# Optimization experiments

Measured on AMD Instinct MI355X. Metric: run time of the kernel, lower is better.

The kernel has to match this reference:

```python
import jax, jax.numpy as jnp
import numpy as np

N_NODES = 500000
N_EDGES = 16000000
F_DIM = 5


def setup_inputs() -> dict:
    key = jax.random.key(0)
    ks = jax.random.split(key, 20)
    inp = {
        "h": jax.random.normal(ks[0], (N_NODES, F_DIM), dtype=jnp.float32),
        "edge_index": jax.random.randint(ks[1], (2, N_EDGES), 0, N_NODES, dtype=jnp.int64),
        "edge_weight": jax.random.uniform(ks[2], (N_EDGES,), dtype=jnp.float32),
    }
    # GCNConv lin weights (bias=False in lin, conv has its own bias) x3
    s = 1.0 / np.sqrt(F_DIM)
    for i in range(3):
        inp[f"W{i+1}"] = jax.random.uniform(ks[3 + i], (F_DIM, F_DIM), jnp.float32, -s, s)
        inp[f"b{i+1}"] = jax.random.uniform(ks[6 + i], (F_DIM,), jnp.float32, -s, s)
    # fc1..fc3 Linear(5,5) with bias
    for i in range(3):
        inp[f"fcW{i+1}"] = jax.random.uniform(ks[9 + i], (F_DIM, F_DIM), jnp.float32, -s, s)
        inp[f"fcb{i+1}"] = jax.random.uniform(ks[12 + i], (F_DIM,), jnp.float32, -s, s)
    return inp


def _gcn_conv(h, src, dst, edge_weight, W, b, num_nodes):
    # lin transform (torch Linear: x @ W.T), no self loops, no normalization
    x = h @ W.T  # [N, F]
    # message: x_j * w_e, gathered from source nodes
    msg = x[src] * edge_weight[:, None]  # [E, F]
    # mean aggregation over target nodes
    agg = jax.ops.segment_sum(msg, dst, num_segments=num_nodes)  # [N, F]
    cnt = jax.ops.segment_sum(jnp.ones_like(edge_weight), dst, num_segments=num_nodes)
    agg = agg / jnp.maximum(cnt, 1.0)[:, None]
    return agg + b


def reference(h, edge_index, edge_weight, W1, b1, W2, b2, W3, b3,
              fcW1, fcb1, fcW2, fcb2, fcW3, fcb3):
    src, dst = edge_index[0], edge_index[1]
    n = h.shape[0]
    for W, b in ((W1, b1), (W2, b2), (W3, b3)):
        h = jax.nn.relu(_gcn_conv(h, src, dst, edge_weight, W, b, n))
    h = jax.nn.relu(h @ fcW1.T + fcb1)
    h = jax.nn.relu(h @ fcW2.T + fcb2)
    h = h @ fcW3.T + fcb3
    return h
```

## Files before the change

kernel.cpp:

```cpp
#include <hip/hip_runtime.h>
#include <hip/hip_fp16.h>


constexpr int N_NODES = 500000;
constexpr int N_EDGES = 16000000;
constexpr int F = 5;
constexpr int NPB = 1024;
constexpr int K_BKT = (N_NODES + NPB - 1) / NPB;
constexpr int CAP = 35008;
constexpr int PART_BLOCKS = 1024;
constexpr int CHUNK = N_EDGES / PART_BLOCKS;
constexpr int SUB = 3125;
constexpr int ACH = 4096;

__global__ void k_init(unsigned* __restrict__ gtail) {
    int b = blockIdx.x * blockDim.x + threadIdx.x;
    if (b < K_BKT) gtail[b] = (unsigned)(b * CAP);
}

__global__ __launch_bounds__(512) void k_part(const int* __restrict__ src,
                                              const int* __restrict__ dst,
                                              const float* __restrict__ ew,
                                              unsigned* __restrict__ gtail,
                                              uint2* __restrict__ sorted) {
    __shared__ uint2 stage[SUB];
    __shared__ unsigned short sbkt[SUB];
    __shared__ unsigned hcnt[512];
    __shared__ unsigned scn[512];
    __shared__ unsigned gb2[512];
    const int t = threadIdx.x;
    const int base_e = blockIdx.x * CHUNK;

#pragma unroll 1
    for (int rnd = 0; rnd < CHUNK / SUB; ++rnd) {
        const int sub_lo = base_e + rnd * SUB;
        hcnt[t] = 0;
        __syncthreads();
        for (int e = sub_lo + t; e < sub_lo + SUB; e += 512)
            atomicAdd(&hcnt[(unsigned)dst[e] >> 10], 1u);
        __syncthreads();
        scn[t] = hcnt[t];
        __syncthreads();
        for (int d = 1; d < 512; d <<= 1) {
            unsigned add = (t >= d) ? scn[t - d] : 0u;
            __syncthreads();
            scn[t] += add;
            __syncthreads();
        }
        unsigned cnt = hcnt[t];
        scn[t] -= cnt;
        if (t < K_BKT && cnt)
            gb2[t] = atomicAdd(&gtail[t], cnt) - scn[t];
        __syncthreads();
        hcnt[t] = 0;
        __syncthreads();
        for (int e = sub_lo + t; e < sub_lo + SUB; e += 512) {
            unsigned d = (unsigned)__builtin_nontemporal_load(dst + e);
            unsigned bkt = d >> 10;
            unsigned p = scn[bkt] + atomicAdd(&hcnt[bkt], 1u);
            uint2 pay;
            pay.x = (unsigned)__builtin_nontemporal_load(src + e) | ((d & (NPB - 1u)) << 19);
            pay.y = __float_as_uint(__builtin_nontemporal_load(ew + e));
            stage[p] = pay;
            sbkt[p] = (unsigned short)bkt;
        }
        __syncthreads();
        for (int p = t; p < SUB; p += 512)
            sorted[gb2[sbkt[p]] + p] = stage[p];
        __syncthreads();
    }
}

__device__ __forceinline__ uint4 pack5(const float o[F]) {
    __half2 p01 = __floats2half2_rn(o[0], o[1]);
    __half2 p23 = __floats2half2_rn(o[2], o[3]);
    __half2 p4z = __floats2half2_rn(o[4], 0.f);
    uint4 pk;
    pk.x = *(const unsigned*)&p01;
    pk.y = *(const unsigned*)&p23;
    pk.z = *(const unsigned*)&p4z;
    pk.w = 0u;
    return pk;
}

__global__ void k_lin(const float* __restrict__ h, const float* __restrict__ W,
                      uint4* __restrict__ x) {
    int i = blockIdx.x * blockDim.x + threadIdx.x;
    if (i >= N_NODES) return;
    float hv[F], o[F];
#pragma unroll
    for (int k = 0; k < F; ++k) hv[k] = h[i * F + k];
#pragma unroll
    for (int f = 0; f < F; ++f) {
        float acc = 0.f;
#pragma unroll
        for (int k = 0; k < F; ++k) acc = fmaf(hv[k], W[f * F + k], acc);
        o[f] = acc;
    }
    x[i] = pack5(o);
}

__device__ __forceinline__ void accum_bucket(const unsigned long long* __restrict__ sorted,
                                             unsigned lo, unsigned hi,
                                             const uint4* __restrict__ x,
                                             unsigned long long* __restrict__ stage,
                                             unsigned* __restrict__ cnt,
                                             unsigned* __restrict__ excl,
                                             unsigned* __restrict__ wsum,
                                             float acc[F], float& deg) {
    const int t = threadIdx.x;
    const int wid = t >> 6, lane = t & 63;
    for (unsigned cb = lo; cb < hi; cb += ACH) {
        const unsigned n = min((unsigned)ACH, hi - cb);
        cnt[t] = 0;
        __syncthreads();
        unsigned long long pe[4];
        unsigned dl[4], rk[4];
#pragma unroll
        for (int i = 0; i < 4; ++i) {
            unsigned idx = (unsigned)t + i * 1024u;
            if (idx < n) {
                pe[i] = __builtin_nontemporal_load(sorted + cb + idx);
                dl[i] = ((unsigned)pe[i]) >> 19;
                rk[i] = atomicAdd(&cnt[dl[i]], 1u);
            }
        }
        __syncthreads();
        unsigned c = cnt[t];
        unsigned inc = c;
#pragma unroll
        for (int d = 1; d < 64; d <<= 1) {
            unsigned up = __shfl_up(inc, d);
            if (lane >= d) inc += up;
        }
        if (lane == 63) wsum[wid] = inc;
        __syncthreads();
        unsigned wbase = 0;
#pragma unroll
        for (int wv = 0; wv < 15; ++wv)
            if (wv < wid) wbase += wsum[wv];
        unsigned my_excl = wbase + inc - c;
        excl[t] = my_excl;
        __syncthreads();
#pragma unroll
        for (int i = 0; i < 4; ++i) {
            unsigned idx = (unsigned)t + i * 1024u;
            if (idx < n) stage[excl[dl[i]] + rk[i]] = pe[i];
        }
        __syncthreads();
        deg += (float)c;
        for (unsigned i = 0; i < c; ++i) {
            unsigned long long e = stage[my_excl + i];
            unsigned px = (unsigned)e;
            float w = __uint_as_float((unsigned)(e >> 32));
            uint4 v = x[px & 0x7FFFFu];
            float2 f01 = __half22float2(*reinterpret_cast<const __half2*>(&v.x));
            float2 f23 = __half22float2(*reinterpret_cast<const __half2*>(&v.y));
            float2 f4z = __half22float2(*reinterpret_cast<const __half2*>(&v.z));
            acc[0] = fmaf(f01.x, w, acc[0]);
            acc[1] = fmaf(f01.y, w, acc[1]);
            acc[2] = fmaf(f23.x, w, acc[2]);
            acc[3] = fmaf(f23.y, w, acc[3]);
            acc[4] = fmaf(f4z.x, w, acc[4]);
        }
        __syncthreads();
    }
}

__global__ __launch_bounds__(1024) void k_gacc(const unsigned long long* __restrict__ sorted,
                                               const unsigned* __restrict__ gtail,
                                               const uint4* __restrict__ x,
                                               const float* __restrict__ bias,
                                               const float* __restrict__ Wn,
                                               uint4* __restrict__ xn) {
    __shared__ unsigned long long stage[ACH];
    __shared__ unsigned cnt[NPB];
    __shared__ unsigned excl[NPB];
    __shared__ unsigned wsum[16];
    float acc[F] = {0.f, 0.f, 0.f, 0.f, 0.f};
    float deg = 0.f;
    const unsigned b = blockIdx.x;
    accum_bucket(sorted, b * CAP, gtail[b], x, stage, cnt, excl, wsum, acc, deg);
    int node = b * NPB + threadIdx.x;
    if (node < N_NODES) {
        float inv = 1.0f / fmaxf(deg, 1.0f);
        float hv[F], o[F];
#pragma unroll
        for (int f = 0; f < F; ++f) hv[f] = fmaxf(fmaf(acc[f], inv, bias[f]), 0.f);
#pragma unroll
        for (int f = 0; f < F; ++f) {
            float s = 0.f;
#pragma unroll
            for (int kk = 0; kk < F; ++kk) s = fmaf(hv[kk], Wn[f * F + kk], s);
            o[f] = s;
        }
        xn[node] = pack5(o);
    }
}

__global__ __launch_bounds__(1024) void k_gfinal(const unsigned long long* __restrict__ sorted,
                                                 const unsigned* __restrict__ gtail,
                                                 const uint4* __restrict__ x,
                                                 const float* __restrict__ b3,
                                                 const float* __restrict__ fcW1, const float* __restrict__ fcb1,
                                                 const float* __restrict__ fcW2, const float* __restrict__ fcb2,
                                                 const float* __restrict__ fcW3, const float* __restrict__ fcb3,
                                                 float* __restrict__ out) {
    __shared__ unsigned long long stage[ACH];
    __shared__ unsigned cnt[NPB];
    __shared__ unsigned excl[NPB];
    __shared__ unsigned wsum[16];
    float acc[F] = {0.f, 0.f, 0.f, 0.f, 0.f};
    float deg = 0.f;
    const unsigned b = blockIdx.x;
    accum_bucket(sorted, b * CAP, gtail[b], x, stage, cnt, excl, wsum, acc, deg);
    int node = b * NPB + threadIdx.x;
    if (node < N_NODES) {
        float inv = 1.0f / fmaxf(deg, 1.0f);
        float h3[F], t1[F], t2[F];
#pragma unroll
        for (int f = 0; f < F; ++f) h3[f] = fmaxf(fmaf(acc[f], inv, b3[f]), 0.f);
#pragma unroll
        for (int f = 0; f < F; ++f) {
            float s = fcb1[f];
#pragma unroll
            for (int kk = 0; kk < F; ++kk) s = fmaf(h3[kk], fcW1[f * F + kk], s);
            t1[f] = fmaxf(s, 0.f);
        }
#pragma unroll
        for (int f = 0; f < F; ++f) {
            float s = fcb2[f];
#pragma unroll
            for (int kk = 0; kk < F; ++kk) s = fmaf(t1[kk], fcW2[f * F + kk], s);
            t2[f] = fmaxf(s, 0.f);
        }
#pragma unroll
        for (int f = 0; f < F; ++f) {
            float s = fcb3[f];
#pragma unroll
            for (int kk = 0; kk < F; ++kk) s = fmaf(t2[kk], fcW3[f * F + kk], s);
            out[node * F + f] = s;
        }
    }
}

extern "C" void kernel_launch(void* const* d_in, const int* in_sizes, int n_in,
                              void* d_out, int out_size, void* d_ws, size_t ws_size,
                              hipStream_t stream) {
    const float* h    = (const float*)d_in[0];
    const int*   ei   = (const int*)d_in[1];
    const float* ew   = (const float*)d_in[2];
    const float* W1   = (const float*)d_in[3];
    const float* b1   = (const float*)d_in[4];
    const float* W2   = (const float*)d_in[5];
    const float* b2   = (const float*)d_in[6];
    const float* W3   = (const float*)d_in[7];
    const float* b3   = (const float*)d_in[8];
    const float* fcW1 = (const float*)d_in[9];
    const float* fcb1 = (const float*)d_in[10];
    const float* fcW2 = (const float*)d_in[11];
    const float* fcb2 = (const float*)d_in[12];
    const float* fcW3 = (const float*)d_in[13];
    const float* fcb3 = (const float*)d_in[14];
    float* out = (float*)d_out;

    const int* srcp = ei;
    const int* dstp = ei + N_EDGES;

    char* ws = (char*)d_ws;
    const size_t MiB = 1024 * 1024;
    unsigned* gtail   = (unsigned*)(ws + 0);
    uint4*    xA      = (uint4*)(ws + 1 * MiB);
    uint4*    xB      = (uint4*)(ws + 10 * MiB);
    uint2*    sorted  = (uint2*)(ws + 19 * MiB);
    const unsigned long long* sorted64 = (const unsigned long long*)sorted;

    dim3 gn((N_NODES + 255) / 256);

    k_init<<<1, 512, 0, stream>>>(gtail);
    k_part<<<PART_BLOCKS, 512, 0, stream>>>(srcp, dstp, ew, gtail, sorted);

    k_lin<<<gn, 256, 0, stream>>>(h, W1, xA);
    k_gacc<<<K_BKT, 1024, 0, stream>>>(sorted64, gtail, xA, b1, W2, xB);
    k_gacc<<<K_BKT, 1024, 0, stream>>>(sorted64, gtail, xB, b2, W3, xA);
    k_gfinal<<<K_BKT, 1024, 0, stream>>>(sorted64, gtail, xA, b3,
                                         fcW1, fcb1, fcW2, fcb2, fcW3, fcb3, out);
}
```

Measured before the change: 934.1 us.

## Build per-node CSR once and use thread-per-node gather for all layers

Adds a second sorting pass that orders each destination bucket's edges by node and records per-node offset and count. All three aggregation layers then use a simple thread-per-node gather over contiguous edges instead of redoing a shared-memory counting sort in every layer. This removes repeated per-layer sorting and atomics. It costs an extra full read and write of the edge array, needs a larger workspace, and per-thread strided edge reads are less coalesced.

```diff
diff --git a/kernel.cpp b/kernel.cpp
--- a/kernel.cpp
+++ b/kernel.cpp
@@ -12,6 +12,7 @@
 constexpr int CHUNK = N_EDGES / PART_BLOCKS;
 constexpr int SUB = 3125;
 constexpr int ACH = 4096;
+constexpr int ACC_BLOCKS = (N_NODES + 255) / 256;
 
 __global__ void k_init(unsigned* __restrict__ gtail) {
     int b = blockIdx.x * blockDim.x + threadIdx.x;
@@ -71,6 +72,69 @@
     }
 }
 
+__global__ __launch_bounds__(1024) void k_sort2(const unsigned long long* __restrict__ in,
+                                                const unsigned* __restrict__ gtail,
+                                                uint2* __restrict__ nodeoff,
+                                                unsigned long long* __restrict__ out) {
+    __shared__ unsigned cnt[NPB];
+    __shared__ unsigned excl[NPB];
+    __shared__ unsigned wsum[16];
+    const int t = threadIdx.x;
+    const int wid = t >> 6, lane = t & 63;
+    const unsigned b = blockIdx.x;
+    const unsigned lo = b * CAP, hi = gtail[b];
+    cnt[t] = 0;
+    __syncthreads();
+    for (unsigned e = lo + t; e < hi; e += 1024) {
+        unsigned long long pe = __builtin_nontemporal_load(in + e);
+        atomicAdd(&cnt[((unsigned)pe) >> 19], 1u);
+    }
+    __syncthreads();
+    unsigned c = cnt[t];
+    unsigned inc = c;
+#pragma unroll
+    for (int d = 1; d < 64; d <<= 1) {
+        unsigned up = __shfl_up(inc, d);
+        if (lane >= d) inc += up;
+    }
+    if (lane == 63) wsum[wid] = inc;
+    __syncthreads();
+    unsigned wbase = 0;
+#pragma unroll
+    for (int wv = 0; wv < 15; ++wv)
+        if (wv < wid) wbase += wsum[wv];
+    unsigned my_excl = wbase + inc - c;
+    excl[t] = my_excl;
+    int node = (int)(b * NPB) + t;
+    if (node < N_NODES) nodeoff[node] = make_uint2(lo + my_excl, c);
+    __syncthreads();
+    cnt[t] = 0;
+    __syncthreads();
+    unsigned e = lo + t;
+    for (; e + 3072 < hi; e += 4096) {
+        unsigned long long p0 = __builtin_nontemporal_load(in + e);
+        unsigned long long p1 = __builtin_nontemporal_load(in + e + 1024);
+        unsigned long long p2 = __builtin_nontemporal_load(in + e + 2048);
+        unsigned long long p3 = __builtin_nontemporal_load(in + e + 3072);
+        unsigned d0 = ((unsigned)p0) >> 19, d1 = ((unsigned)p1) >> 19;
+        unsigned d2 = ((unsigned)p2) >> 19, d3 = ((unsigned)p3) >> 19;
+        unsigned q0 = excl[d0] + atomicAdd(&cnt[d0], 1u);
+        unsigned q1 = excl[d1] + atomicAdd(&cnt[d1], 1u);
+        unsigned q2 = excl[d2] + atomicAdd(&cnt[d2], 1u);
+        unsigned q3 = excl[d3] + atomicAdd(&cnt[d3], 1u);
+        out[lo + q0] = p0;
+        out[lo + q1] = p1;
+        out[lo + q2] = p2;
+        out[lo + q3] = p3;
+    }
+    for (; e < hi; e += 1024) {
+        unsigned long long p0 = __builtin_nontemporal_load(in + e);
+        unsigned d0 = ((unsigned)p0) >> 19;
+        unsigned q0 = excl[d0] + atomicAdd(&cnt[d0], 1u);
+        out[lo + q0] = p0;
+    }
+}
+
 __device__ __forceinline__ uint4 pack5(const float o[F]) {
     __half2 p01 = __floats2half2_rn(o[0], o[1]);
     __half2 p23 = __floats2half2_rn(o[2], o[3]);
@@ -98,6 +162,109 @@
         o[f] = acc;
     }
     x[i] = pack5(o);
+}
+
+__device__ __forceinline__ void fma_edge(unsigned long long pe, const uint4& v,
+                                         float acc[F]) {
+    float w = __uint_as_float((unsigned)(pe >> 32));
+    float2 f01 = __half22float2(*reinterpret_cast<const __half2*>(&v.x));
+    float2 f23 = __half22float2(*reinterpret_cast<const __half2*>(&v.y));
+    float2 f4z = __half22float2(*reinterpret_cast<const __half2*>(&v.z));
+    acc[0] = fmaf(f01.x, w, acc[0]);
+    acc[1] = fmaf(f01.y, w, acc[1]);
+    acc[2] = fmaf(f23.x, w, acc[2]);
+    acc[3] = fmaf(f23.y, w, acc[3]);
+    acc[4] = fmaf(f4z.x, w, acc[4]);
+}
+
+__device__ __forceinline__ void node_accum(const unsigned long long* __restrict__ s2,
+                                           uint2 oc, const uint4* __restrict__ x,
+                                           float acc[F]) {
+    unsigned i = 0;
+    for (; i + 4 <= oc.y; i += 4) {
+        unsigned long long e0 = s2[oc.x + i];
+        unsigned long long e1 = s2[oc.x + i + 1];
+        unsigned long long e2 = s2[oc.x + i + 2];
+        unsigned long long e3 = s2[oc.x + i + 3];
+        uint4 v0 = x[(unsigned)e0 & 0x7FFFFu];
+        uint4 v1 = x[(unsigned)e1 & 0x7FFFFu];
+        uint4 v2 = x[(unsigned)e2 & 0x7FFFFu];
+        uint4 v3 = x[(unsigned)e3 & 0x7FFFFu];
+        fma_edge(e0, v0, acc);
+        fma_edge(e1, v1, acc);
+        fma_edge(e2, v2, acc);
+        fma_edge(e3, v3, acc);
+    }
+    for (; i < oc.y; ++i) {
+        unsigned long long e0 = s2[oc.x + i];
+        uint4 v0 = x[(unsigned)e0 & 0x7FFFFu];
+        fma_edge(e0, v0, acc);
+    }
+}
+
+__global__ __launch_bounds__(256) void k_gacc2(const unsigned long long* __restrict__ s2,
+                                               const uint2* __restrict__ nodeoff,
+                                               const uint4* __restrict__ x,
+                                               const float* __restrict__ bias,
+                                               const float* __restrict__ Wn,
+                                               uint4* __restrict__ xn) {
+    int node = blockIdx.x * 256 + threadIdx.x;
+    if (node >= N_NODES) return;
+    uint2 oc = nodeoff[node];
+    float acc[F] = {0.f, 0.f, 0.f, 0.f, 0.f};
+    node_accum(s2, oc, x, acc);
+    float inv = 1.0f / fmaxf((float)oc.y, 1.0f);
+    float hv[F], o[F];
+#pragma unroll
+    for (int f = 0; f < F; ++f) hv[f] = fmaxf(fmaf(acc[f], inv, bias[f]), 0.f);
+#pragma unroll
+    for (int f = 0; f < F; ++f) {
+        float s = 0.f;
+#pragma unroll
+        for (int kk = 0; kk < F; ++kk) s = fmaf(hv[kk], Wn[f * F + kk], s);
+        o[f] = s;
+    }
+    xn[node] = pack5(o);
+}
+
+__global__ __launch_bounds__(256) void k_gfinal2(const unsigned long long* __restrict__ s2,
+                                                 const uint2* __restrict__ nodeoff,
+                                                 const uint4* __restrict__ x,
+                                                 const float* __restrict__ b3,
+                                                 const float* __restrict__ fcW1, const float* __restrict__ fcb1,
+                                                 const float* __restrict__ fcW2, const float* __restrict__ fcb2,
+                                                 const float* __restrict__ fcW3, const float* __restrict__ fcb3,
+                                                 float* __restrict__ out) {
+    int node = blockIdx.x * 256 + threadIdx.x;
+    if (node >= N_NODES) return;
+    uint2 oc = nodeoff[node];
+    float acc[F] = {0.f, 0.f, 0.f, 0.f, 0.f};
+    node_accum(s2, oc, x, acc);
+    float inv = 1.0f / fmaxf((float)oc.y, 1.0f);
+    float h3[F], t1[F], t2[F];
+#pragma unroll
+    for (int f = 0; f < F; ++f) h3[f] = fmaxf(fmaf(acc[f], inv, b3[f]), 0.f);
+#pragma unroll
+    for (int f = 0; f < F; ++f) {
+        float s = fcb1[f];
+#pragma unroll
+        for (int kk = 0; kk < F; ++kk) s = fmaf(h3[kk], fcW1[f * F + kk], s);
+        t1[f] = fmaxf(s, 0.f);
+    }
+#pragma unroll
+    for (int f = 0; f < F; ++f) {
+        float s = fcb2[f];
+#pragma unroll
+        for (int kk = 0; kk < F; ++kk) s = fmaf(t1[kk], fcW2[f * F + kk], s);
+        t2[f] = fmaxf(s, 0.f);
+    }
+#pragma unroll
+    for (int f = 0; f < F; ++f) {
+        float s = fcb3[f];
+#pragma unroll
+        for (int kk = 0; kk < F; ++kk) s = fmaf(t2[kk], fcW3[f * F + kk], s);
+        out[node * F + f] = s;
+    }
 }
 
 __device__ __forceinline__ void accum_bucket(const unsigned long long* __restrict__ sorted,
@@ -269,20 +436,33 @@
 
     char* ws = (char*)d_ws;
     const size_t MiB = 1024 * 1024;
+    const size_t SORT_BYTES = (size_t)K_BKT * CAP * 8;
     unsigned* gtail   = (unsigned*)(ws + 0);
     uint4*    xA      = (uint4*)(ws + 1 * MiB);
     uint4*    xB      = (uint4*)(ws + 10 * MiB);
-    uint2*    sorted  = (uint2*)(ws + 19 * MiB);
+    uint2*    nodeoff = (uint2*)(ws + 18 * MiB);
+    uint2*    sorted  = (uint2*)(ws + 22 * MiB);
+    unsigned long long* sorted2 =
+        (unsigned long long*)(ws + 153 * MiB);
     const unsigned long long* sorted64 = (const unsigned long long*)sorted;
+    const size_t NEED = 153 * MiB + SORT_BYTES;
 
     dim3 gn((N_NODES + 255) / 256);
 
     k_init<<<1, 512, 0, stream>>>(gtail);
     k_part<<<PART_BLOCKS, 512, 0, stream>>>(srcp, dstp, ew, gtail, sorted);
-
     k_lin<<<gn, 256, 0, stream>>>(h, W1, xA);
-    k_gacc<<<K_BKT, 1024, 0, stream>>>(sorted64, gtail, xA, b1, W2, xB);
-    k_gacc<<<K_BKT, 1024, 0, stream>>>(sorted64, gtail, xB, b2, W3, xA);
-    k_gfinal<<<K_BKT, 1024, 0, stream>>>(sorted64, gtail, xA, b3,
-                                         fcW1, fcb1, fcW2, fcb2, fcW3, fcb3, out);
-}
+
+    if (ws_size >= NEED) {
+        k_sort2<<<K_BKT, 1024, 0, stream>>>(sorted64, gtail, nodeoff, sorted2);
+        k_gacc2<<<ACC_BLOCKS, 256, 0, stream>>>(sorted2, nodeoff, xA, b1, W2, xB);
+        k_gacc2<<<ACC_BLOCKS, 256, 0, stream>>>(sorted2, nodeoff, xB, b2, W3, xA);
+        k_gfinal2<<<ACC_BLOCKS, 256, 0, stream>>>(sorted2, nodeoff, xA, b3,
+                                                  fcW1, fcb1, fcW2, fcb2, fcW3, fcb3, out);
+    } else {
+        k_gacc<<<K_BKT, 1024, 0, stream>>>(sorted64, gtail, xA, b1, W2, xB);
+        k_gacc<<<K_BKT, 1024, 0, stream>>>(sorted64, gtail, xB, b2, W3, xA);
+        k_gfinal<<<K_BKT, 1024, 0, stream>>>(sorted64, gtail, xA, b3,
+                                             fcW1, fcb1, fcW2, fcb2, fcW3, fcb3, out);
+    }
+}
```

Result: slower. 1.382 ms (+48.0%).

## Prefetch next edge chunk during local sort and unroll gather loop by four

Applied to the files above, without the earlier changes.

The per-bucket accumulation now loads the next chunk of sorted edges into registers while the current chunk is being scattered into shared memory. It also unrolls the per-node gather loop four ways so four x loads are in flight at once. Chunk size grows from 4096 to 6144 edges, the partition grid is set to 1000 blocks of 4000 sub-chunks, and the count and prefix arrays share one shared-memory buffer. The extra registers for six prefetched edges plus the unrolled loads raise register pressure, and the larger stage uses more LDS, both of which can cut occupancy.

```diff
diff --git a/kernel.cpp b/kernel.cpp
--- a/kernel.cpp
+++ b/kernel.cpp
@@ -8,10 +8,10 @@
 constexpr int NPB = 1024;
 constexpr int K_BKT = (N_NODES + NPB - 1) / NPB;
 constexpr int CAP = 35008;
-constexpr int PART_BLOCKS = 1024;
+constexpr int PART_BLOCKS = 1000;
 constexpr int CHUNK = N_EDGES / PART_BLOCKS;
-constexpr int SUB = 3125;
-constexpr int ACH = 4096;
+constexpr int SUB = 4000;
+constexpr int ACH = 6144;
 
 __global__ void k_init(unsigned* __restrict__ gtail) {
     int b = blockIdx.x * blockDim.x + threadIdx.x;
@@ -100,33 +100,51 @@
     x[i] = pack5(o);
 }
 
+__device__ __forceinline__ void fma_edge(unsigned long long pe, const uint4& v,
+                                         float acc[F]) {
+    float w = __uint_as_float((unsigned)(pe >> 32));
+    float2 f01 = __half22float2(*reinterpret_cast<const __half2*>(&v.x));
+    float2 f23 = __half22float2(*reinterpret_cast<const __half2*>(&v.y));
+    float2 f4z = __half22float2(*reinterpret_cast<const __half2*>(&v.z));
+    acc[0] = fmaf(f01.x, w, acc[0]);
+    acc[1] = fmaf(f01.y, w, acc[1]);
+    acc[2] = fmaf(f23.x, w, acc[2]);
+    acc[3] = fmaf(f23.y, w, acc[3]);
+    acc[4] = fmaf(f4z.x, w, acc[4]);
+}
+
 __device__ __forceinline__ void accum_bucket(const unsigned long long* __restrict__ sorted,
                                              unsigned lo, unsigned hi,
                                              const uint4* __restrict__ x,
                                              unsigned long long* __restrict__ stage,
-                                             unsigned* __restrict__ cnt,
-                                             unsigned* __restrict__ excl,
+                                             unsigned* __restrict__ cntx,
                                              unsigned* __restrict__ wsum,
                                              float acc[F], float& deg) {
     const int t = threadIdx.x;
     const int wid = t >> 6, lane = t & 63;
+    unsigned long long pe[6];
+    bool val[6];
+    {
+        unsigned n0 = hi - lo;
+        if (n0 > (unsigned)ACH) n0 = ACH;
+#pragma unroll
+        for (int i = 0; i < 6; ++i) {
+            unsigned idx = (unsigned)t + i * 1024u;
+            val[i] = idx < n0;
+            pe[i] = val[i] ? __builtin_nontemporal_load(sorted + lo + idx) : 0ull;
+        }
+    }
     for (unsigned cb = lo; cb < hi; cb += ACH) {
-        const unsigned n = min((unsigned)ACH, hi - cb);
-        cnt[t] = 0;
-        __syncthreads();
-        unsigned long long pe[4];
-        unsigned dl[4], rk[4];
-#pragma unroll
-        for (int i = 0; i < 4; ++i) {
-            unsigned idx = (unsigned)t + i * 1024u;
-            if (idx < n) {
-                pe[i] = __builtin_nontemporal_load(sorted + cb + idx);
-                dl[i] = ((unsigned)pe[i]) >> 19;
-                rk[i] = atomicAdd(&cnt[dl[i]], 1u);
-            }
-        }
-        __syncthreads();
-        unsigned c = cnt[t];
+        cntx[t] = 0;
+        __syncthreads();
+        unsigned dl[6], rk[6];
+#pragma unroll
+        for (int i = 0; i < 6; ++i) {
+            dl[i] = ((unsigned)pe[i]) >> 19;
+            if (val[i]) rk[i] = atomicAdd(&cntx[dl[i]], 1u);
+        }
+        __syncthreads();
+        unsigned c = cntx[t];
         unsigned inc = c;
 #pragma unroll
         for (int d = 1; d < 64; d <<= 1) {
@@ -140,28 +158,43 @@
         for (int wv = 0; wv < 15; ++wv)
             if (wv < wid) wbase += wsum[wv];
         unsigned my_excl = wbase + inc - c;
-        excl[t] = my_excl;
-        __syncthreads();
-#pragma unroll
-        for (int i = 0; i < 4; ++i) {
-            unsigned idx = (unsigned)t + i * 1024u;
-            if (idx < n) stage[excl[dl[i]] + rk[i]] = pe[i];
+        cntx[t] = my_excl;
+        __syncthreads();
+#pragma unroll
+        for (int i = 0; i < 6; ++i)
+            if (val[i]) stage[cntx[dl[i]] + rk[i]] = pe[i];
+        {
+            unsigned cb2 = cb + ACH;
+            unsigned n2 = (cb2 < hi) ? (hi - cb2) : 0u;
+            if (n2 > (unsigned)ACH) n2 = ACH;
+#pragma unroll
+            for (int i = 0; i < 6; ++i) {
+                unsigned idx = (unsigned)t + i * 1024u;
+                val[i] = idx < n2;
+                pe[i] = val[i] ? __builtin_nontemporal_load(sorted + cb2 + idx) : 0ull;
+            }
         }
         __syncthreads();
         deg += (float)c;
-        for (unsigned i = 0; i < c; ++i) {
-            unsigned long long e = stage[my_excl + i];
-            unsigned px = (unsigned)e;
-            float w = __uint_as_float((unsigned)(e >> 32));
-            uint4 v = x[px & 0x7FFFFu];
-            float2 f01 = __half22float2(*reinterpret_cast<const __half2*>(&v.x));
-            float2 f23 = __half22float2(*reinterpret_cast<const __half2*>(&v.y));
-            float2 f4z = __half22float2(*reinterpret_cast<const __half2*>(&v.z));
-            acc[0] = fmaf(f01.x, w, acc[0]);
-            acc[1] = fmaf(f01.y, w, acc[1]);
-            acc[2] = fmaf(f23.x, w, acc[2]);
-            acc[3] = fmaf(f23.y, w, acc[3]);
-            acc[4] = fmaf(f4z.x, w, acc[4]);
+        unsigned i = 0;
+        for (; i + 4 <= c; i += 4) {
+            unsigned long long e0 = stage[my_excl + i];
+            unsigned long long e1 = stage[my_excl + i + 1];
+            unsigned long long e2 = stage[my_excl + i + 2];
+            unsigned long long e3 = stage[my_excl + i + 3];
+            uint4 v0 = x[(unsigned)e0 & 0x7FFFFu];
+            uint4 v1 = x[(unsigned)e1 & 0x7FFFFu];
+            uint4 v2 = x[(unsigned)e2 & 0x7FFFFu];
+            uint4 v3 = x[(unsigned)e3 & 0x7FFFFu];
+            fma_edge(e0, v0, acc);
+            fma_edge(e1, v1, acc);
+            fma_edge(e2, v2, acc);
+            fma_edge(e3, v3, acc);
+        }
+        for (; i < c; ++i) {
+            unsigned long long e0 = stage[my_excl + i];
+            uint4 v0 = x[(unsigned)e0 & 0x7FFFFu];
+            fma_edge(e0, v0, acc);
         }
         __syncthreads();
     }
@@ -174,13 +207,12 @@
                                                const float* __restrict__ Wn,
                                                uint4* __restrict__ xn) {
     __shared__ unsigned long long stage[ACH];
-    __shared__ unsigned cnt[NPB];
-    __shared__ unsigned excl[NPB];
+    __shared__ unsigned cntx[NPB];
     __shared__ unsigned wsum[16];
     float acc[F] = {0.f, 0.f, 0.f, 0.f, 0.f};
     float deg = 0.f;
     const unsigned b = blockIdx.x;
-    accum_bucket(sorted, b * CAP, gtail[b], x, stage, cnt, excl, wsum, acc, deg);
+    accum_bucket(sorted, b * CAP, gtail[b], x, stage, cntx, wsum, acc, deg);
     int node = b * NPB + threadIdx.x;
     if (node < N_NODES) {
         float inv = 1.0f / fmaxf(deg, 1.0f);
@@ -207,13 +239,12 @@
                                                  const float* __restrict__ fcW3, const float* __restrict__ fcb3,
                                                  float* __restrict__ out) {
     __shared__ unsigned long long stage[ACH];
-    __shared__ unsigned cnt[NPB];
-    __shared__ unsigned excl[NPB];
+    __shared__ unsigned cntx[NPB];
     __shared__ unsigned wsum[16];
     float acc[F] = {0.f, 0.f, 0.f, 0.f, 0.f};
     float deg = 0.f;
     const unsigned b = blockIdx.x;
-    accum_bucket(sorted, b * CAP, gtail[b], x, stage, cnt, excl, wsum, acc, deg);
+    accum_bucket(sorted, b * CAP, gtail[b], x, stage, cntx, wsum, acc, deg);
     int node = b * NPB + threadIdx.x;
     if (node < N_NODES) {
         float inv = 1.0f / fmaxf(deg, 1.0f);
```

Result: faster. 895.9 us (-4.1%).
